# Kernel optimization log

Measured on AMD Instinct MI355X. Metric: run time of the kernel, lower is better.

## Reference

```python
import jax, jax.numpy as jnp
import numpy as np

B, NH, T, N = 8, 12, 1024, 256
THETA = 2.0 ** 16
TWO_PI = 2.0 * np.pi


def make_freqs(n, theta):
    # RoPE frequencies in cycles (phases_cos_sin later does %1 * 2*pi)
    half = theta ** (-np.arange(0, n, 2, dtype=np.float64) / n) / TWO_PI
    return jnp.asarray(np.repeat(half, 2), dtype=jnp.float32).reshape(1, 1, 1, n)


def setup_inputs() -> dict:
    key = jax.random.key(0)
    kq, kv = jax.random.split(key)
    Q = jax.random.normal(kq, (B, NH, T, N), dtype=jnp.float32)
    V = jax.random.normal(kv, (B, NH, T, N), dtype=jnp.float32)
    return {"Q": Q, "V": V, "freqs": make_freqs(N, THETA)}


def rope(phases, v):
    ang = (phases % 1.0) * (2.0 * jnp.pi)
    cos, sin = jnp.cos(ang), jnp.sin(ang)
    # pair rotation: (even, odd) -> (-odd, even)
    v_rot = jnp.stack((-v[..., 1::2], v[..., ::2]), axis=-1).reshape(v.shape)
    return v * cos + v_rot * sin


def reference(Q, V, freqs):
    t = Q.shape[2]
    # phases: [1,1,T,1] * [1,1,1,N] -> [1,1,T,N]
    phases = jnp.arange(t, dtype=freqs.dtype).reshape(1, 1, -1, 1) * freqs
    QR = rope(phases, Q)  # KR = QR (K is Q)
    scores = jnp.einsum('bhtn,bhsn->bhts', QR, QR)
    scale = jnp.asarray(Q.shape[-1], Q.dtype) ** 0.5
    attn = jax.nn.softmax(scores / scale, axis=-1)
    return jnp.einsum('bhts,bhsn->bhtn', attn, V)
```

## Files before the change

kernel.cpp:

```cpp
#include <hip/hip_runtime.h>
#include <hip/hip_bf16.h>
#include <stdint.h>

#define B_ 8
#define NH_ 12
#define NBH (B_*NH_)
#define T_ 1024
#define D_ 256
#define GRP 48
#define NG (NBH/GRP)
#define G1BLK (GRP*8*8)
#define G2BLK (GRP*8*2)

typedef __attribute__((ext_vector_type(8))) short bf16x8;
typedef __attribute__((ext_vector_type(16))) float f32x16;
typedef unsigned short ushort_t;

#define Z16 ((f32x16){0,0,0,0,0,0,0,0,0,0,0,0,0,0,0,0})

#define KSCALE 0.30028060218f

__device__ __forceinline__ short f2bf(float x) {
  __hip_bfloat16 h = __float2bfloat16(x);
  return *reinterpret_cast<short*>(&h);
}
__device__ __forceinline__ float bf2f(short x) {
  unsigned int u = ((unsigned int)(unsigned short)x) << 16;
  return __uint_as_float(u);
}
__device__ __forceinline__ void gload16(const ushort_t* g, ushort_t* l) {
  __builtin_amdgcn_global_load_lds(
      (const __attribute__((address_space(1))) uint32_t*)g,
      (__attribute__((address_space(3))) uint32_t*)l, 16, 0, 0);
}


__global__ void tab_kernel(const float* __restrict__ freqs, float2* __restrict__ tab) {
  int idx = blockIdx.x * blockDim.x + threadIdx.x;
  if (idx >= T_ * (D_/2)) return;
  int t = idx >> 7;
  int i = idx & 127;
  float ph = (float)t * freqs[2*i];
  ph -= floorf(ph);
  float ang = ph * 6.283185307179586f;
  tab[idx] = make_float2(cosf(ang), sinf(ang));
}

__global__ __launch_bounds__(256) void kr_kernel(const float* __restrict__ Q,
                                                 const float2* __restrict__ tab,
                                                 ushort_t* __restrict__ KR) {
  int row = blockIdx.x * 8 + (threadIdx.x >> 5);
  int d8  = threadIdx.x & 31;
  int t = row & (T_ - 1);
  const float* src = Q + (size_t)row * D_ + d8 * 8;
  float4 x0 = *(const float4*)src;
  float4 x1 = *(const float4*)(src + 4);
  const float2* tr = tab + t * (D_/2) + d8 * 4;
  float2 c0 = tr[0], c1 = tr[1], c2 = tr[2], c3 = tr[3];
  bf16x8 f;
  f[0] = f2bf((x0.x * c0.x - x0.y * c0.y) * KSCALE);
  f[1] = f2bf((x0.y * c0.x + x0.x * c0.y) * KSCALE);
  f[2] = f2bf((x0.z * c1.x - x0.w * c1.y) * KSCALE);
  f[3] = f2bf((x0.w * c1.x + x0.z * c1.y) * KSCALE);
  f[4] = f2bf((x1.x * c2.x - x1.y * c2.y) * KSCALE);
  f[5] = f2bf((x1.y * c2.x + x1.x * c2.y) * KSCALE);
  f[6] = f2bf((x1.z * c3.x - x1.w * c3.y) * KSCALE);
  f[7] = f2bf((x1.w * c3.x + x1.z * c3.y) * KSCALE);
  *(bf16x8*)(KR + (size_t)row * D_ + d8 * 8) = f;
}

__global__ __launch_bounds__(256) void vt_kernel(const float* __restrict__ V,
                                                 ushort_t* __restrict__ VT) {
  int blk = blockIdx.x;
  int d64 = blk & 3, t64 = (blk >> 2) & 15, bh = blk >> 6;
  __shared__ ushort_t st[64][66];
  {
    int t = threadIdx.x >> 2, j = threadIdx.x & 3;
    const float* src = V + ((size_t)bh * T_ + t64 * 64 + t) * D_ + d64 * 64 + j * 16;
#pragma unroll
    for (int q2 = 0; q2 < 4; ++q2) {
      float4 x = *(const float4*)(src + q2 * 4);
      st[t][j*16 + q2*4 + 0] = (ushort_t)f2bf(x.x);
      st[t][j*16 + q2*4 + 1] = (ushort_t)f2bf(x.y);
      st[t][j*16 + q2*4 + 2] = (ushort_t)f2bf(x.z);
      st[t][j*16 + q2*4 + 3] = (ushort_t)f2bf(x.w);
    }
  }
  __syncthreads();
  {
    int d = threadIdx.x >> 2, tq = threadIdx.x & 3;
    bf16x8 a_, b_;
#pragma unroll
    for (int i = 0; i < 8; ++i) {
      a_[i] = (short)st[tq*16 + i][d];
      b_[i] = (short)st[tq*16 + 8 + i][d];
    }
    ushort_t* dst = VT + ((size_t)bh * D_ + d64*64 + d) * T_ + t64*64 + tq*16;
    *(bf16x8*)dst = a_;
    *(bf16x8*)(dst + 8) = b_;
  }
}

__global__ __launch_bounds__(256, 4)
void gemm1_kernel(const ushort_t* __restrict__ KRg, ushort_t* __restrict__ P) {
  int bid = blockIdx.x;
  int swz = (bid & 7) * (G1BLK / 8) + (bid >> 3);
  int si = swz & 7;
  int ti = (swz >> 3) & 7;
  int h  = swz >> 6;

  const ushort_t* __restrict__ Kh = KRg + (size_t)h * (T_ * D_);
  ushort_t* __restrict__ Ph = P + (size_t)h * (T_ * T_);

  const int tid = threadIdx.x, lane = tid & 63, wv = tid >> 6;
  const int lo = lane & 31, hi = lane >> 5;

  __shared__ __align__(16) ushort_t At[128 * 64];
  __shared__ __align__(16) ushort_t Bt[128 * 64];

  f32x16 acc[4];
#pragma unroll
  for (int j = 0; j < 4; ++j) acc[j] = Z16;

  const ushort_t* Abase = Kh + (size_t)ti * 128 * D_;
  const ushort_t* Bbase = Kh + (size_t)si * 128 * D_;

  for (int ks = 0; ks < 4; ++ks) {
    int k0 = ks * 64;
    __syncthreads();
#pragma unroll
    for (int i = 0; i < 4; ++i) {
      int d = tid + i * 256;
      int r = d >> 3, c = d & 7;
      int srcoff = r * D_ + k0 + ((c ^ (r & 7)) * 8);
      gload16(Abase + srcoff, &At[d * 8]);
      gload16(Bbase + srcoff, &Bt[d * 8]);
    }
    __syncthreads();
    __builtin_amdgcn_s_setprio(1);
#pragma unroll
    for (int kk = 0; kk < 4; ++kk) {
      int ra = 32 * wv + lo;
      bf16x8 af = *(const bf16x8*)&At[ra * 64 + (((2*kk + hi) ^ (ra & 7)) * 8)];
#pragma unroll
      for (int j = 0; j < 4; ++j) {
        int rb = 32 * j + lo;
        bf16x8 bf_ = *(const bf16x8*)&Bt[rb * 64 + (((2*kk + hi) ^ (rb & 7)) * 8)];
        acc[j] = __builtin_amdgcn_mfma_f32_32x32x16_bf16(af, bf_, acc[j], 0, 0, 0);
      }
    }
    __builtin_amdgcn_s_setprio(0);
  }

#pragma unroll
  for (int j = 0; j < 4; ++j) {
#pragma unroll
    for (int r = 0; r < 16; ++r) {
      int t = ti * 128 + 32 * wv + ((r & 3) + 8 * (r >> 2) + 4 * hi);
      int s = si * 128 + 32 * j + lo;
      Ph[(size_t)t * T_ + s] = (ushort_t)f2bf(exp2f(acc[j][r]));
    }
  }
}

__global__ __launch_bounds__(256, 4)
void gemm2_kernel(const ushort_t* __restrict__ P, const ushort_t* __restrict__ VTg,
                  float* __restrict__ Og) {
  int bid = blockIdx.x;
  int swz = (bid & 7) * (G2BLK / 8) + (bid >> 3);
  int di = swz & 1;
  int ti = (swz >> 1) & 7;
  int h  = swz >> 4;

  const ushort_t* __restrict__ Ph = P + (size_t)h * (T_ * T_);
  const ushort_t* __restrict__ Vh = VTg + (size_t)h * (D_ * T_);
  float* __restrict__ Oh = Og + (size_t)h * (T_ * D_);

  const int tid = threadIdx.x, lane = tid & 63, wv = tid >> 6;
  const int lo = lane & 31, hi = lane >> 5;

  __shared__ __align__(16) ushort_t At[128 * 64];
  __shared__ __align__(16) ushort_t Bt[128 * 64];
  __shared__ float lB[4][32];

  f32x16 acc[4];
#pragma unroll
  for (int j = 0; j < 4; ++j) acc[j] = Z16;
  float lsum = 0.0f;

  const ushort_t* Abase = Ph + (size_t)ti * 128 * T_;
  const ushort_t* Bbase = Vh + (size_t)di * 128 * T_;

  for (int ks = 0; ks < 16; ++ks) {
    int k0 = ks * 64;
    __syncthreads();
#pragma unroll
    for (int i = 0; i < 4; ++i) {
      int d = tid + i * 256;
      int r = d >> 3, c = d & 7;
      int srcoff = r * T_ + k0 + ((c ^ (r & 7)) * 8);
      gload16(Abase + srcoff, &At[d * 8]);
      gload16(Bbase + srcoff, &Bt[d * 8]);
    }
    __syncthreads();
    __builtin_amdgcn_s_setprio(1);
#pragma unroll
    for (int kk = 0; kk < 4; ++kk) {
      int ra = 32 * wv + lo;
      bf16x8 pf = *(const bf16x8*)&At[ra * 64 + (((2*kk + hi) ^ (ra & 7)) * 8)];
      float s01 = bf2f(pf[0]) + bf2f(pf[1]);
      float s23 = bf2f(pf[2]) + bf2f(pf[3]);
      float s45 = bf2f(pf[4]) + bf2f(pf[5]);
      float s67 = bf2f(pf[6]) + bf2f(pf[7]);
      lsum += (s01 + s23) + (s45 + s67);
#pragma unroll
      for (int j = 0; j < 4; ++j) {
        int rb = 32 * j + lo;
        bf16x8 vf = *(const bf16x8*)&Bt[rb * 64 + (((2*kk + hi) ^ (rb & 7)) * 8)];
        acc[j] = __builtin_amdgcn_mfma_f32_32x32x16_bf16(pf, vf, acc[j], 0, 0, 0);
      }
    }
    __builtin_amdgcn_s_setprio(0);
  }

  lsum += __shfl_xor(lsum, 32);
  if (hi == 0) lB[wv][lo] = lsum;
  asm volatile("s_waitcnt lgkmcnt(0)" ::: "memory");

#pragma unroll
  for (int r = 0; r < 16; ++r) {
    int crow = (r & 3) + 8 * (r >> 2) + 4 * hi;
    float inv = 1.0f / lB[wv][crow];
    int t = ti * 128 + 32 * wv + crow;
#pragma unroll
    for (int j = 0; j < 4; ++j) {
      Oh[(size_t)t * D_ + di * 128 + 32 * j + lo] = acc[j][r] * inv;
    }
  }
}

extern "C" void kernel_launch(void* const* d_in, const int* in_sizes, int n_in,
                              void* d_out, int out_size, void* d_ws, size_t ws_size,
                              hipStream_t stream) {
  const float* Q     = (const float*)d_in[0];
  const float* V     = (const float*)d_in[1];
  const float* freqs = (const float*)d_in[2];
  float* Out = (float*)d_out;

  float2* tab  = (float2*)d_ws;
  ushort_t* KR = (ushort_t*)((char*)d_ws + (1 << 20));
  ushort_t* VT = (ushort_t*)((char*)d_ws + (1 << 20) + (size_t)NBH * T_ * D_ * 2);
  ushort_t* P  = (ushort_t*)((char*)d_ws + (1 << 20) + (size_t)2 * NBH * T_ * D_ * 2);

  tab_kernel<<<(T_ * (D_/2) + 255) / 256, 256, 0, stream>>>(freqs, tab);
  kr_kernel<<<NBH * T_ / 8, 256, 0, stream>>>(Q, tab, KR);
  vt_kernel<<<NBH * 16 * 4, 256, 0, stream>>>(V, VT);

  for (int g = 0; g < NG; ++g) {
    const ushort_t* KRg = KR + (size_t)g * GRP * T_ * D_;
    const ushort_t* VTg = VT + (size_t)g * GRP * D_ * T_;
    float* Og = Out + (size_t)g * GRP * T_ * D_;
    gemm1_kernel<<<G1BLK, 256, 0, stream>>>(KRg, P);
    gemm2_kernel<<<G2BLK, 256, 0, stream>>>(P, VTg, Og);
  }
}
```

Measured before the change: 262.0 us.

## Exploit score symmetry: compute lower-triangle tiles and mirror-transpose into P

Because K equals Q, the score matrix is symmetric, so gemm1 now computes only the 36 lower-triangle 128x128 tiles per head instead of 64. Each off-diagonal tile is also written transposed through LDS to fill the mirror tile. The launch also uses a single group of all heads when the workspace is large enough, which cuts kernel launches and improves occupancy. The cost is extra LDS transpose work and stores, a sqrt-based tile index decode, and reliance on the workspace size.

```diff
diff --git a/kernel.cpp b/kernel.cpp
--- a/kernel.cpp
+++ b/kernel.cpp
@@ -7,10 +7,6 @@
 #define NBH (B_*NH_)
 #define T_ 1024
 #define D_ 256
-#define GRP 48
-#define NG (NBH/GRP)
-#define G1BLK (GRP*8*8)
-#define G2BLK (GRP*8*2)
 
 typedef __attribute__((ext_vector_type(8))) short bf16x8;
 typedef __attribute__((ext_vector_type(16))) float f32x16;
@@ -104,10 +100,12 @@
 __global__ __launch_bounds__(256, 4)
 void gemm1_kernel(const ushort_t* __restrict__ KRg, ushort_t* __restrict__ P) {
   int bid = blockIdx.x;
-  int swz = (bid & 7) * (G1BLK / 8) + (bid >> 3);
-  int si = swz & 7;
-  int ti = (swz >> 3) & 7;
-  int h  = swz >> 6;
+  int nblk = gridDim.x;
+  int swz = (bid & 7) * (nblk >> 3) + (bid >> 3);
+  int b = swz % 36;
+  int h = swz / 36;
+  int ti = (int)((sqrtf(8.0f * b + 1.0f) - 1.0f) * 0.5f);
+  int si = b - ti * (ti + 1) / 2;
 
   const ushort_t* __restrict__ Kh = KRg + (size_t)h * (T_ * D_);
   ushort_t* __restrict__ Ph = P + (size_t)h * (T_ * T_);
@@ -115,8 +113,9 @@
   const int tid = threadIdx.x, lane = tid & 63, wv = tid >> 6;
   const int lo = lane & 31, hi = lane >> 5;
 
-  __shared__ __align__(16) ushort_t At[128 * 64];
-  __shared__ __align__(16) ushort_t Bt[128 * 64];
+  __shared__ __align__(16) ushort_t SH[2 * 128 * 64];
+  ushort_t* At = SH;
+  ushort_t* Bt = SH + 128 * 64;
 
   f32x16 acc[4];
 #pragma unroll
@@ -152,13 +151,43 @@
     __builtin_amdgcn_s_setprio(0);
   }
 
+  ushort_t pe[4][16];
+#pragma unroll
+  for (int j = 0; j < 4; ++j)
+#pragma unroll
+    for (int r = 0; r < 16; ++r)
+      pe[j][r] = (ushort_t)f2bf(exp2f(acc[j][r]));
+
 #pragma unroll
   for (int j = 0; j < 4; ++j) {
 #pragma unroll
     for (int r = 0; r < 16; ++r) {
       int t = ti * 128 + 32 * wv + ((r & 3) + 8 * (r >> 2) + 4 * hi);
       int s = si * 128 + 32 * j + lo;
-      Ph[(size_t)t * T_ + s] = (ushort_t)f2bf(exp2f(acc[j][r]));
+      Ph[(size_t)t * T_ + s] = pe[j][r];
+    }
+  }
+
+  if (ti != si) {
+    __syncthreads();
+    ushort_t* Lt = SH;
+#pragma unroll
+    for (int j = 0; j < 4; ++j) {
+#pragma unroll
+      for (int r = 0; r < 16; ++r) {
+        int trow = 32 * wv + ((r & 3) + 8 * (r >> 2) + 4 * hi);
+        int scol = 32 * j + lo;
+        int cc = (trow >> 3) ^ (scol & 7);
+        Lt[scol * 128 + (cc << 3) + (trow & 7)] = pe[j][r];
+      }
+    }
+    __syncthreads();
+#pragma unroll
+    for (int it = 0; it < 8; ++it) {
+      int sr = it * 16 + (tid >> 4);
+      int c  = tid & 15;
+      bf16x8 vv = *(const bf16x8*)&Lt[sr * 128 + ((c ^ (sr & 7)) << 3)];
+      *(bf16x8*)&Ph[(size_t)(si * 128 + sr) * T_ + ti * 128 + c * 8] = vv;
     }
   }
 }
@@ -167,7 +196,8 @@
 void gemm2_kernel(const ushort_t* __restrict__ P, const ushort_t* __restrict__ VTg,
                   float* __restrict__ Og) {
   int bid = blockIdx.x;
-  int swz = (bid & 7) * (G2BLK / 8) + (bid >> 3);
+  int nblk = gridDim.x;
+  int swz = (bid & 7) * (nblk >> 3) + (bid >> 3);
   int di = swz & 1;
   int ti = (swz >> 1) & 7;
   int h  = swz >> 4;
@@ -256,11 +286,16 @@
   kr_kernel<<<NBH * T_ / 8, 256, 0, stream>>>(Q, tab, KR);
   vt_kernel<<<NBH * 16 * 4, 256, 0, stream>>>(V, VT);
 
-  for (int g = 0; g < NG; ++g) {
-    const ushort_t* KRg = KR + (size_t)g * GRP * T_ * D_;
-    const ushort_t* VTg = VT + (size_t)g * GRP * D_ * T_;
-    float* Og = Out + (size_t)g * GRP * T_ * D_;
-    gemm1_kernel<<<G1BLK, 256, 0, stream>>>(KRg, P);
-    gemm2_kernel<<<G2BLK, 256, 0, stream>>>(P, VTg, Og);
-  }
-}
+  size_t base = (1 << 20) + (size_t)2 * NBH * T_ * D_ * 2;
+  size_t need1 = base + (size_t)NBH * T_ * T_ * 2;
+  int ng = (ws_size >= need1) ? 1 : 2;
+  int hg = NBH / ng;
+
+  for (int g = 0; g < ng; ++g) {
+    const ushort_t* KRg = KR + (size_t)g * hg * T_ * D_;
+    const ushort_t* VTg = VT + (size_t)g * hg * D_ * T_;
+    float* Og = Out + (size_t)g * hg * T_ * D_;
+    gemm1_kernel<<<hg * 36, 256, 0, stream>>>(KRg, P);
+    gemm2_kernel<<<hg * 16, 256, 0, stream>>>(P, VTg, Og);
+  }
+}
```

New measurement: 235.8 us. -10.0%, faster.
